# Kernel tuning notes

Measured on AMD Instinct MI355X. Metric: run time of the kernel, lower is better.

## Reference

```python
import jax, jax.numpy as jnp
import numpy as np

N_NODES = 50000
N_EDGES = 500000
D_IN = 768
D_H = 512
BN_EPS = 1e-5


def _gin_conv(x, src, dst, W1, b1, gamma, beta, rmean, rvar, W2, b2):
    # GINConv (eps=0): h_i = MLP((1+0)*x_i + sum_{j->i} x_j)
    agg = jax.ops.segment_sum(x[src], dst, num_segments=N_NODES)  # [N, d]
    h = x + agg
    h = h @ W1 + b1
    # BatchNorm1d in eval mode with running stats
    h = (h - rmean) * jax.lax.rsqrt(rvar + BN_EPS) * gamma + beta
    h = jax.nn.relu(h)
    h = jax.nn.relu(h @ W2 + b2)
    return h


def setup_inputs() -> dict:
    key = jax.random.key(0)
    ks = jax.random.split(key, 12)
    x = jax.random.normal(ks[0], (N_NODES, D_IN), dtype=jnp.float32)
    edge_index = jax.random.randint(ks[1], (2, N_EDGES), 0, N_NODES, dtype=jnp.int64)

    def lin(k, fan_in, fan_out):
        kw, kb = jax.random.split(k)
        bound = 1.0 / np.sqrt(fan_in)
        W = jax.random.uniform(kw, (fan_in, fan_out), minval=-bound, maxval=bound, dtype=jnp.float32)
        b = jax.random.uniform(kb, (fan_out,), minval=-bound, maxval=bound, dtype=jnp.float32)
        return W, b

    W1a, b1a = lin(ks[2], D_IN, D_H)
    W1b, b1b = lin(ks[3], D_H, D_H)
    W2a, b2a = lin(ks[4], D_H, D_H)
    W2b, b2b = lin(ks[5], D_H, D_H)
    Wout, bout = lin(ks[6], D_H, 2)

    return {
        "x": x, "edge_index": edge_index,
        "W1a": W1a, "b1a": b1a,
        "bn1_gamma": jnp.ones((D_H,), jnp.float32), "bn1_beta": jnp.zeros((D_H,), jnp.float32),
        "bn1_mean": jnp.zeros((D_H,), jnp.float32), "bn1_var": jnp.ones((D_H,), jnp.float32),
        "W1b": W1b, "b1b": b1b,
        "W2a": W2a, "b2a": b2a,
        "bn2_gamma": jnp.ones((D_H,), jnp.float32), "bn2_beta": jnp.zeros((D_H,), jnp.float32),
        "bn2_mean": jnp.zeros((D_H,), jnp.float32), "bn2_var": jnp.ones((D_H,), jnp.float32),
        "W2b": W2b, "b2b": b2b,
        "Wout": Wout, "bout": bout,
    }


def reference(x, edge_index,
              W1a, b1a, bn1_gamma, bn1_beta, bn1_mean, bn1_var, W1b, b1b,
              W2a, b2a, bn2_gamma, bn2_beta, bn2_mean, bn2_var, W2b, b2b,
              Wout, bout):
    src, dst = edge_index[0], edge_index[1]
    h1 = _gin_conv(x, src, dst, W1a, b1a, bn1_gamma, bn1_beta, bn1_mean, bn1_var, W1b, b1b)
    h2 = _gin_conv(h1, src, dst, W2a, b2a, bn2_gamma, bn2_beta, bn2_mean, bn2_var, W2b, b2b)
    h = h2 @ Wout + bout  # [N, 2]
    # dropout p=0.5 is identity in eval mode
    return h
```

## Files before the change

### kernel.cpp

```cpp
#include <hip/hip_runtime.h>

typedef short short8  __attribute__((ext_vector_type(8)));
typedef short short4v __attribute__((ext_vector_type(4)));
typedef float f32x4   __attribute__((ext_vector_type(4)));

__device__ __forceinline__ short f2bf(float f) {
  union { float f; unsigned u; } v; v.f = f;
  unsigned r = v.u + 0x7fffu + ((v.u >> 16) & 1u);
  return (short)(r >> 16);
}

__device__ __forceinline__ void gload_lds16(const short* g, short* l) {
  __builtin_amdgcn_global_load_lds(
      (const __attribute__((address_space(1))) void*)g,
      (__attribute__((address_space(3))) void*)l, 16, 0, 0);
}

template <int EPI>
__launch_bounds__(256)
__global__ void gemm_bt(const short* __restrict__ A, const short* __restrict__ Bt,
                        float* __restrict__ Cf, short* __restrict__ Cb,
                        int Mpad, int N, int K,
                        const float* __restrict__ bias,
                        const float* __restrict__ gamma, const float* __restrict__ beta,
                        const float* __restrict__ mean, const float* __restrict__ var) {
  __shared__ short lA[128 * 32];
  __shared__ short lB[128 * 32];
  const int t = threadIdx.x;
  const int lane = t & 63;
  const int wave = t >> 6;
  const int wr = (wave >> 1) * 64;
  const int wc = (wave & 1) * 64;
  const int tileM = blockIdx.y * 128;
  const int tileN = blockIdx.x * 128;

  f32x4 acc[4][4] = {};

  const short* aSrc = A  + (size_t)(tileM + (t >> 2)) * K + (t & 3) * 8;
  const short* bSrc = Bt + (size_t)(tileN + (t >> 2)) * K + (t & 3) * 8;
  const size_t rowStep = (size_t)64 * K;
  short* lAdst = lA + t * 8;
  short* lBdst = lB + t * 8;

  const int fr = lane & 15;
  const int kg = (lane >> 4) * 8;

  for (int k0 = 0; k0 < K; k0 += 32) {
    gload_lds16(aSrc + k0,           lAdst);
    gload_lds16(aSrc + rowStep + k0, lAdst + 64 * 32);
    gload_lds16(bSrc + k0,           lBdst);
    gload_lds16(bSrc + rowStep + k0, lBdst + 64 * 32);
    __syncthreads();
    short8 af[4], bf[4];
#pragma unroll
    for (int m = 0; m < 4; ++m)
      af[m] = *(const short8*)(lA + (wr + m * 16 + fr) * 32 + kg);
#pragma unroll
    for (int n = 0; n < 4; ++n)
      bf[n] = *(const short8*)(lB + (wc + n * 16 + fr) * 32 + kg);
#pragma unroll
    for (int m = 0; m < 4; ++m)
#pragma unroll
      for (int n = 0; n < 4; ++n)
        acc[m][n] = __builtin_amdgcn_mfma_f32_16x16x32_bf16(af[m], bf[n], acc[m][n], 0, 0, 0);
    __syncthreads();
  }

  const int rg = (lane >> 4) * 4;
#pragma unroll
  for (int m = 0; m < 4; ++m) {
#pragma unroll
    for (int n = 0; n < 4; ++n) {
      const int col = tileN + wc + n * 16 + fr;
      const float bi = (EPI >= 1) ? bias[col] : 0.f;
      float sc = 1.f, sh = 0.f;
      if (EPI == 2) {
        sc = rsqrtf(var[col] + 1e-5f) * gamma[col];
        sh = beta[col] - mean[col] * sc;
      }
#pragma unroll
      for (int r = 0; r < 4; ++r) {
        const int row = tileM + wr + m * 16 + rg + r;
        float v = acc[m][n][r] + bi;
        if (EPI == 2) v = v * sc + sh;
        if (EPI >= 1) v = fmaxf(v, 0.f);
        if (EPI == 2) Cb[(size_t)row * N + col] = f2bf(v);
        else          Cf[(size_t)row * N + col] = v;
      }
    }
  }
}

__global__ void conv_x_bf(const float* __restrict__ x, short* __restrict__ xb,
                          long nReal, long nTot) {
  long i = ((long)blockIdx.x * blockDim.x + threadIdx.x) * 4;
  if (i >= nTot) return;
  short4v o;
  if (i < nReal) {
    o[0] = f2bf(x[i + 0]); o[1] = f2bf(x[i + 1]);
    o[2] = f2bf(x[i + 2]); o[3] = f2bf(x[i + 3]);
  } else {
    o[0] = o[1] = o[2] = o[3] = 0;
  }
  *(short4v*)(xb + i) = o;
}

__global__ void conv_w_t(const float* __restrict__ W, short* __restrict__ Wt, int K, int N) {
  int idx = blockIdx.x * blockDim.x + threadIdx.x;
  if (idx >= K * N) return;
  int k = idx / N, n = idx - k * N;
  Wt[(size_t)n * K + k] = f2bf(W[idx]);
}

__global__ void hist_deg(const int* __restrict__ dst, int* __restrict__ deg, int nE) {
  int e = blockIdx.x * blockDim.x + threadIdx.x;
  if (e < nE) atomicAdd(&deg[dst[e]], 1);
}

__global__ void scan_deg(const int* __restrict__ deg, int* __restrict__ rowstart,
                         int* __restrict__ cursor, int n) {
  __shared__ int wsum[16];
  __shared__ int carrySh;
  const int t = threadIdx.x;
  const int lane = t & 63, wv = t >> 6;
  int carry = 0;
  for (int base = 0; base < n; base += 8192) {
    int v[8]; int s = 0;
    const int i0 = base + t * 8;
#pragma unroll
    for (int j = 0; j < 8; ++j) {
      int idx = i0 + j;
      v[j] = (idx < n) ? deg[idx] : 0;
      s += v[j];
    }
    int ps = s;
#pragma unroll
    for (int off = 1; off < 64; off <<= 1) {
      int u = __shfl_up(ps, off);
      if (lane >= off) ps += u;
    }
    if (lane == 63) wsum[wv] = ps;
    __syncthreads();
    if (wv == 0 && lane < 16) {
      int wsv = wsum[lane];
      int pw = wsv;
#pragma unroll
      for (int off = 1; off < 16; off <<= 1) {
        int u = __shfl_up(pw, off);
        if (lane >= off) pw += u;
      }
      wsum[lane] = pw - wsv;
      if (lane == 15) carrySh = pw;
    }
    __syncthreads();
    int run = carry + wsum[wv] + (ps - s);
#pragma unroll
    for (int j = 0; j < 8; ++j) {
      int idx = i0 + j;
      if (idx < n) { rowstart[idx] = run; cursor[idx] = run; }
      run += v[j];
    }
    carry += carrySh;
    __syncthreads();
  }
  if (t == 0) rowstart[n] = carry;
}

__global__ void fill_adj(const int* __restrict__ src, const int* __restrict__ dst,
                         int* __restrict__ cursor, int* __restrict__ adj, int nE) {
  int e = blockIdx.x * blockDim.x + threadIdx.x;
  if (e < nE) {
    int p = atomicAdd(&cursor[dst[e]], 1);
    adj[p] = src[e];
  }
}

template <int EPI>
__launch_bounds__(256)
__global__ void agg_csr(const float* __restrict__ Y,
                        const int* __restrict__ rowstart, const int* __restrict__ adj,
                        const float* __restrict__ bias, const float* __restrict__ gm,
                        const float* __restrict__ bt, const float* __restrict__ mn,
                        const float* __restrict__ vr,
                        short* __restrict__ out, int M) {
  const int node = blockIdx.x * 4 + (threadIdx.x >> 6);
  if (node >= M) return;
  const int lane = threadIdx.x & 63;
  const int d0 = lane * 8;

  const float* yr = Y + (size_t)node * 512 + d0;
  f32x4 a0 = *(const f32x4*)yr;
  f32x4 a1 = *(const f32x4*)(yr + 4);

  int s = rowstart[node];
  const int e = rowstart[node + 1];
  while (s < e) {
    const int cnt = min(e - s, 64);
    int myn = (lane < cnt) ? adj[s + lane] : 0;
    int i = 0;
    for (; i + 1 < cnt; i += 2) {
      int n0 = __shfl(myn, i);
      int n1 = __shfl(myn, i + 1);
      const float* r0 = Y + (size_t)n0 * 512 + d0;
      const float* r1 = Y + (size_t)n1 * 512 + d0;
      f32x4 b0 = *(const f32x4*)r0;
      f32x4 b1 = *(const f32x4*)(r0 + 4);
      f32x4 c0 = *(const f32x4*)r1;
      f32x4 c1 = *(const f32x4*)(r1 + 4);
      a0 += b0; a1 += b1; a0 += c0; a1 += c1;
    }
    if (i < cnt) {
      int n0 = __shfl(myn, i);
      const float* r0 = Y + (size_t)n0 * 512 + d0;
      a0 += *(const f32x4*)r0;
      a1 += *(const f32x4*)(r0 + 4);
    }
    s += cnt;
  }

  short8 o;
#pragma unroll
  for (int j = 0; j < 8; ++j) {
    float val = (j < 4) ? a0[j] : a1[j - 4];
    if (EPI == 1) {
      const int d = d0 + j;
      float sc = rsqrtf(vr[d] + 1e-5f) * gm[d];
      float tv = (val + bias[d] - mn[d]) * sc + bt[d];
      o[j] = f2bf(fmaxf(tv, 0.f));
    } else {
      o[j] = f2bf(val);
    }
  }
  *(short8*)(out + (size_t)node * 512 + d0) = o;
}

__global__ void out_proj(const float* __restrict__ H, const float* __restrict__ Wout,
                         const float* __restrict__ bout, float* __restrict__ out, int M) {
  int row = blockIdx.x * 4 + (threadIdx.x >> 6);
  if (row >= M) return;
  int lane = threadIdx.x & 63;
  const float* hr = H + (size_t)row * 512;
  float s0 = 0.f, s1 = 0.f;
#pragma unroll
  for (int i = 0; i < 8; ++i) {
    float h = hr[lane + i * 64];
    s0 += h * Wout[(lane + i * 64) * 2 + 0];
    s1 += h * Wout[(lane + i * 64) * 2 + 1];
  }
#pragma unroll
  for (int off = 32; off > 0; off >>= 1) {
    s0 += __shfl_down(s0, off);
    s1 += __shfl_down(s1, off);
  }
  if (lane == 0) {
    out[row * 2 + 0] = s0 + bout[0];
    out[row * 2 + 1] = s1 + bout[1];
  }
}

extern "C" void kernel_launch(void* const* d_in, const int* in_sizes, int n_in,
                              void* d_out, int out_size, void* d_ws, size_t ws_size,
                              hipStream_t stream) {
  const float* x   = (const float*)d_in[0];
  const int*   ei  = (const int*)d_in[1];
  const float* W1a = (const float*)d_in[2];
  const float* b1a = (const float*)d_in[3];
  const float* g1  = (const float*)d_in[4];
  const float* be1 = (const float*)d_in[5];
  const float* m1  = (const float*)d_in[6];
  const float* v1  = (const float*)d_in[7];
  const float* W1b = (const float*)d_in[8];
  const float* b1b = (const float*)d_in[9];
  const float* W2a = (const float*)d_in[10];
  const float* b2a = (const float*)d_in[11];
  const float* g2  = (const float*)d_in[12];
  const float* be2 = (const float*)d_in[13];
  const float* m2  = (const float*)d_in[14];
  const float* v2  = (const float*)d_in[15];
  const float* W2b = (const float*)d_in[16];
  const float* b2b = (const float*)d_in[17];
  const float* Wo  = (const float*)d_in[18];
  const float* bo  = (const float*)d_in[19];

  const int DH   = in_sizes[3];
  const int DIN  = in_sizes[2] / DH;
  const int NN   = in_sizes[0] / DIN;
  const int nE   = in_sizes[1] / 2;
  const int Mpad = (NN + 127) & ~127;

  char* ws = (char*)d_ws;
  short* XB = (short*)ws;
  size_t off = (size_t)Mpad * DIN * 2;
  short* W1aT = (short*)(ws + off); off += (size_t)DH * DIN * 2;
  short* W1bT = (short*)(ws + off); off += (size_t)DH * DH * 2;
  short* W2aT = (short*)(ws + off); off += (size_t)DH * DH * 2;
  short* W2bT = (short*)(ws + off); off += (size_t)DH * DH * 2;
  off = (off + 255) & ~(size_t)255;
  float* B1 = (float*)(ws + off); off += (size_t)Mpad * DH * 4;
  short* B3 = (short*)(ws + off); off += (size_t)Mpad * DH * 2;
  off = (off + 255) & ~(size_t)255;
  int* deg      = (int*)(ws + off); off += (size_t)(Mpad + 1) * 4;
  int* rowstart = (int*)(ws + off); off += (size_t)(Mpad + 1) * 4;
  int* cursor   = (int*)(ws + off); off += (size_t)(Mpad + 1) * 4;
  int* adj      = (int*)(ws + off); off += (size_t)nE * 4;

  const int* srcI = ei;
  const int* dstI = ei + nE;

  const long nTot = (long)Mpad * DIN, nReal = (long)NN * DIN;

  conv_x_bf<<<(int)((nTot / 4 + 255) / 256), 256, 0, stream>>>(x, XB, nReal, nTot);
  conv_w_t<<<(DIN * DH + 255) / 256, 256, 0, stream>>>(W1a, W1aT, DIN, DH);
  conv_w_t<<<(DH * DH + 255) / 256, 256, 0, stream>>>(W1b, W1bT, DH, DH);
  conv_w_t<<<(DH * DH + 255) / 256, 256, 0, stream>>>(W2a, W2aT, DH, DH);
  conv_w_t<<<(DH * DH + 255) / 256, 256, 0, stream>>>(W2b, W2bT, DH, DH);
  hipMemsetAsync(deg, 0, (size_t)(Mpad + 1) * 4, stream);
  hist_deg<<<(nE + 255) / 256, 256, 0, stream>>>(dstI, deg, nE);
  scan_deg<<<1, 1024, 0, stream>>>(deg, rowstart, cursor, Mpad);
  fill_adj<<<(nE + 255) / 256, 256, 0, stream>>>(srcI, dstI, cursor, adj, nE);

  dim3 gg(DH / 128, Mpad / 128);
  const int aggGrid = Mpad / 4;

  gemm_bt<0><<<gg, 256, 0, stream>>>(XB, W1aT, B1, nullptr, Mpad, DH, DIN,
                                     nullptr, nullptr, nullptr, nullptr, nullptr);
  agg_csr<1><<<aggGrid, 256, 0, stream>>>(B1, rowstart, adj, b1a, g1, be1, m1, v1, B3, Mpad);
  gemm_bt<1><<<gg, 256, 0, stream>>>(B3, W1bT, B1, nullptr, Mpad, DH, DH,
                                     b1b, nullptr, nullptr, nullptr, nullptr);
  agg_csr<0><<<aggGrid, 256, 0, stream>>>(B1, rowstart, adj, nullptr, nullptr, nullptr,
                                          nullptr, nullptr, B3, Mpad);
  gemm_bt<2><<<gg, 256, 0, stream>>>(B3, W2aT, nullptr, XB, Mpad, DH, DH,
                                     b2a, g2, be2, m2, v2);
  gemm_bt<1><<<gg, 256, 0, stream>>>(XB, W2bT, B1, nullptr, Mpad, DH, DH,
                                     b2b, nullptr, nullptr, nullptr, nullptr);
  out_proj<<<(NN + 3) / 4, 256, 0, stream>>>(B1, Wo, bo, (float*)d_out, NN);
}
```

Measured before the change: 971.6 us.

## Store intermediate GEMM outputs in bf16 to halve gather traffic

GEMM outputs that feed the edge aggregation and output projection are now written as bf16 instead of fp32, so the gather-heavy CSR aggregation reads half the bytes per neighbor row. The aggregation loop is unrolled by four neighbors, and the four weight-transpose launches are merged into one kernel. The extra bf16 rounding before summation adds a small accuracy cost.

```diff
diff --git a/kernel.cpp b/kernel.cpp
--- a/kernel.cpp
+++ b/kernel.cpp
@@ -10,17 +10,22 @@
   return (short)(r >> 16);
 }
 
+__device__ __forceinline__ float bf2f(short s) {
+  union { unsigned u; float f; } v;
+  v.u = ((unsigned)(unsigned short)s) << 16;
+  return v.f;
+}
+
 __device__ __forceinline__ void gload_lds16(const short* g, short* l) {
   __builtin_amdgcn_global_load_lds(
       (const __attribute__((address_space(1))) void*)g,
       (__attribute__((address_space(3))) void*)l, 16, 0, 0);
 }
 
-template <int EPI>
+template <bool BIAS, bool BN, bool RELU>
 __launch_bounds__(256)
 __global__ void gemm_bt(const short* __restrict__ A, const short* __restrict__ Bt,
-                        float* __restrict__ Cf, short* __restrict__ Cb,
-                        int Mpad, int N, int K,
+                        short* __restrict__ C, int Mpad, int N, int K,
                         const float* __restrict__ bias,
                         const float* __restrict__ gamma, const float* __restrict__ beta,
                         const float* __restrict__ mean, const float* __restrict__ var) {
@@ -72,9 +77,9 @@
 #pragma unroll
     for (int n = 0; n < 4; ++n) {
       const int col = tileN + wc + n * 16 + fr;
-      const float bi = (EPI >= 1) ? bias[col] : 0.f;
+      const float bi = BIAS ? bias[col] : 0.f;
       float sc = 1.f, sh = 0.f;
-      if (EPI == 2) {
+      if (BN) {
         sc = rsqrtf(var[col] + 1e-5f) * gamma[col];
         sh = beta[col] - mean[col] * sc;
       }
@@ -82,10 +87,9 @@
       for (int r = 0; r < 4; ++r) {
         const int row = tileM + wr + m * 16 + rg + r;
         float v = acc[m][n][r] + bi;
-        if (EPI == 2) v = v * sc + sh;
-        if (EPI >= 1) v = fmaxf(v, 0.f);
-        if (EPI == 2) Cb[(size_t)row * N + col] = f2bf(v);
-        else          Cf[(size_t)row * N + col] = v;
+        if (BN) v = v * sc + sh;
+        if (RELU) v = fmaxf(v, 0.f);
+        C[(size_t)row * N + col] = f2bf(v);
       }
     }
   }
@@ -105,11 +109,26 @@
   *(short4v*)(xb + i) = o;
 }
 
-__global__ void conv_w_t(const float* __restrict__ W, short* __restrict__ Wt, int K, int N) {
+__global__ void conv_w_all(const float* __restrict__ W1a, const float* __restrict__ W1b,
+                           const float* __restrict__ W2a, const float* __restrict__ W2b,
+                           short* __restrict__ W1aT, short* __restrict__ W1bT,
+                           short* __restrict__ W2aT, short* __restrict__ W2bT,
+                           int DIN, int DH) {
   int idx = blockIdx.x * blockDim.x + threadIdx.x;
-  if (idx >= K * N) return;
-  int k = idx / N, n = idx - k * N;
-  Wt[(size_t)n * K + k] = f2bf(W[idx]);
+  const int n1 = DIN * DH, n2 = DH * DH;
+  if (idx < n1) {
+    int k = idx / DH, n = idx - k * DH;
+    W1aT[(size_t)n * DIN + k] = f2bf(W1a[idx]);
+    return;
+  }
+  idx -= n1;
+  if (idx >= 3 * n2) return;
+  const int which = idx / n2;
+  const int r = idx - which * n2;
+  const int k = r / DH, n = r - k * DH;
+  const float* W = (which == 0) ? W1b : (which == 1) ? W2a : W2b;
+  short* T = (which == 0) ? W1bT : (which == 1) ? W2aT : W2bT;
+  T[(size_t)n * DH + k] = f2bf(W[r]);
 }
 
 __global__ void hist_deg(const int* __restrict__ dst, int* __restrict__ deg, int nE) {
@@ -175,9 +194,16 @@
   }
 }
 
+__device__ __forceinline__ void addbf8(f32x4& a0, f32x4& a1, short8 v) {
+#pragma unroll
+  for (int j = 0; j < 4; ++j) a0[j] += bf2f(v[j]);
+#pragma unroll
+  for (int j = 0; j < 4; ++j) a1[j] += bf2f(v[4 + j]);
+}
+
 template <int EPI>
 __launch_bounds__(256)
-__global__ void agg_csr(const float* __restrict__ Y,
+__global__ void agg_csr(const short* __restrict__ Y,
                         const int* __restrict__ rowstart, const int* __restrict__ adj,
                         const float* __restrict__ bias, const float* __restrict__ gm,
                         const float* __restrict__ bt, const float* __restrict__ mn,
@@ -188,9 +214,8 @@
   const int lane = threadIdx.x & 63;
   const int d0 = lane * 8;
 
-  const float* yr = Y + (size_t)node * 512 + d0;
-  f32x4 a0 = *(const f32x4*)yr;
-  f32x4 a1 = *(const f32x4*)(yr + 4);
+  f32x4 a0 = {}, a1 = {};
+  addbf8(a0, a1, *(const short8*)(Y + (size_t)node * 512 + d0));
 
   int s = rowstart[node];
   const int e = rowstart[node + 1];
@@ -198,22 +223,21 @@
     const int cnt = min(e - s, 64);
     int myn = (lane < cnt) ? adj[s + lane] : 0;
     int i = 0;
-    for (; i + 1 < cnt; i += 2) {
+    for (; i + 3 < cnt; i += 4) {
       int n0 = __shfl(myn, i);
       int n1 = __shfl(myn, i + 1);
-      const float* r0 = Y + (size_t)n0 * 512 + d0;
-      const float* r1 = Y + (size_t)n1 * 512 + d0;
-      f32x4 b0 = *(const f32x4*)r0;
-      f32x4 b1 = *(const f32x4*)(r0 + 4);
-      f32x4 c0 = *(const f32x4*)r1;
-      f32x4 c1 = *(const f32x4*)(r1 + 4);
-      a0 += b0; a1 += b1; a0 += c0; a1 += c1;
-    }
-    if (i < cnt) {
+      int n2 = __shfl(myn, i + 2);
+      int n3 = __shfl(myn, i + 3);
+      short8 v0 = *(const short8*)(Y + (size_t)n0 * 512 + d0);
+      short8 v1 = *(const short8*)(Y + (size_t)n1 * 512 + d0);
+      short8 v2 = *(const short8*)(Y + (size_t)n2 * 512 + d0);
+      short8 v3 = *(const short8*)(Y + (size_t)n3 * 512 + d0);
+      addbf8(a0, a1, v0); addbf8(a0, a1, v1);
+      addbf8(a0, a1, v2); addbf8(a0, a1, v3);
+    }
+    for (; i < cnt; ++i) {
       int n0 = __shfl(myn, i);
-      const float* r0 = Y + (size_t)n0 * 512 + d0;
-      a0 += *(const f32x4*)r0;
-      a1 += *(const f32x4*)(r0 + 4);
+      addbf8(a0, a1, *(const short8*)(Y + (size_t)n0 * 512 + d0));
     }
     s += cnt;
   }
@@ -234,18 +258,18 @@
   *(short8*)(out + (size_t)node * 512 + d0) = o;
 }
 
-__global__ void out_proj(const float* __restrict__ H, const float* __restrict__ Wout,
+__global__ void out_proj(const short* __restrict__ H, const float* __restrict__ Wout,
                          const float* __restrict__ bout, float* __restrict__ out, int M) {
   int row = blockIdx.x * 4 + (threadIdx.x >> 6);
   if (row >= M) return;
   int lane = threadIdx.x & 63;
-  const float* hr = H + (size_t)row * 512;
+  const short8 v = *(const short8*)(H + (size_t)row * 512 + lane * 8);
   float s0 = 0.f, s1 = 0.f;
 #pragma unroll
-  for (int i = 0; i < 8; ++i) {
-    float h = hr[lane + i * 64];
-    s0 += h * Wout[(lane + i * 64) * 2 + 0];
-    s1 += h * Wout[(lane + i * 64) * 2 + 1];
+  for (int j = 0; j < 8; ++j) {
+    float h = bf2f(v[j]);
+    s0 += h * Wout[(lane * 8 + j) * 2 + 0];
+    s1 += h * Wout[(lane * 8 + j) * 2 + 1];
   }
 #pragma unroll
   for (int off = 32; off > 0; off >>= 1) {
@@ -296,8 +320,8 @@
   short* W2aT = (short*)(ws + off); off += (size_t)DH * DH * 2;
   short* W2bT = (short*)(ws + off); off += (size_t)DH * DH * 2;
   off = (off + 255) & ~(size_t)255;
-  float* B1 = (float*)(ws + off); off += (size_t)Mpad * DH * 4;
-  short* B3 = (short*)(ws + off); off += (size_t)Mpad * DH * 2;
+  short* P = (short*)(ws + off); off += (size_t)Mpad * DH * 2;
+  short* Q = (short*)(ws + off); off += (size_t)Mpad * DH * 2;
   off = (off + 255) & ~(size_t)255;
   int* deg      = (int*)(ws + off); off += (size_t)(Mpad + 1) * 4;
   int* rowstart = (int*)(ws + off); off += (size_t)(Mpad + 1) * 4;
@@ -310,10 +334,8 @@
   const long nTot = (long)Mpad * DIN, nReal = (long)NN * DIN;
 
   conv_x_bf<<<(int)((nTot / 4 + 255) / 256), 256, 0, stream>>>(x, XB, nReal, nTot);
-  conv_w_t<<<(DIN * DH + 255) / 256, 256, 0, stream>>>(W1a, W1aT, DIN, DH);
-  conv_w_t<<<(DH * DH + 255) / 256, 256, 0, stream>>>(W1b, W1bT, DH, DH);
-  conv_w_t<<<(DH * DH + 255) / 256, 256, 0, stream>>>(W2a, W2aT, DH, DH);
-  conv_w_t<<<(DH * DH + 255) / 256, 256, 0, stream>>>(W2b, W2bT, DH, DH);
+  conv_w_all<<<(DIN * DH + 3 * DH * DH + 255) / 256, 256, 0, stream>>>(
+      W1a, W1b, W2a, W2b, W1aT, W1bT, W2aT, W2bT, DIN, DH);
   hipMemsetAsync(deg, 0, (size_t)(Mpad + 1) * 4, stream);
   hist_deg<<<(nE + 255) / 256, 256, 0, stream>>>(dstI, deg, nE);
   scan_deg<<<1, 1024, 0, stream>>>(deg, rowstart, cursor, Mpad);
@@ -322,16 +344,16 @@
   dim3 gg(DH / 128, Mpad / 128);
   const int aggGrid = Mpad / 4;
 
-  gemm_bt<0><<<gg, 256, 0, stream>>>(XB, W1aT, B1, nullptr, Mpad, DH, DIN,
-                                     nullptr, nullptr, nullptr, nullptr, nullptr);
-  agg_csr<1><<<aggGrid, 256, 0, stream>>>(B1, rowstart, adj, b1a, g1, be1, m1, v1, B3, Mpad);
-  gemm_bt<1><<<gg, 256, 0, stream>>>(B3, W1bT, B1, nullptr, Mpad, DH, DH,
-                                     b1b, nullptr, nullptr, nullptr, nullptr);
-  agg_csr<0><<<aggGrid, 256, 0, stream>>>(B1, rowstart, adj, nullptr, nullptr, nullptr,
-                                          nullptr, nullptr, B3, Mpad);
-  gemm_bt<2><<<gg, 256, 0, stream>>>(B3, W2aT, nullptr, XB, Mpad, DH, DH,
-                                     b2a, g2, be2, m2, v2);
-  gemm_bt<1><<<gg, 256, 0, stream>>>(XB, W2bT, B1, nullptr, Mpad, DH, DH,
-                                     b2b, nullptr, nullptr, nullptr, nullptr);
-  out_proj<<<(NN + 3) / 4, 256, 0, stream>>>(B1, Wo, bo, (float*)d_out, NN);
-}
+  gemm_bt<false, false, false><<<gg, 256, 0, stream>>>(XB, W1aT, P, Mpad, DH, DIN,
+                                                       nullptr, nullptr, nullptr, nullptr, nullptr);
+  agg_csr<1><<<aggGrid, 256, 0, stream>>>(P, rowstart, adj, b1a, g1, be1, m1, v1, Q, Mpad);
+  gemm_bt<true, false, true><<<gg, 256, 0, stream>>>(Q, W1bT, P, Mpad, DH, DH,
+                                                     b1b, nullptr, nullptr, nullptr, nullptr);
+  agg_csr<0><<<aggGrid, 256, 0, stream>>>(P, rowstart, adj, nullptr, nullptr, nullptr,
+                                          nullptr, nullptr, Q, Mpad);
+  gemm_bt<true, true, true><<<gg, 256, 0, stream>>>(Q, W2aT, P, Mpad, DH, DH,
+                                                    b2a, g2, be2, m2, v2);
+  gemm_bt<true, false, true><<<gg, 256, 0, stream>>>(P, W2bT, Q, Mpad, DH, DH,
+                                                     b2b, nullptr, nullptr, nullptr, nullptr);
+  out_proj<<<(NN + 3) / 4, 256, 0, stream>>>(Q, Wo, bo, (float*)d_out, NN);
+}
```

Measured after the change: 792.6 us. -18.4%, faster.
